# Kernel tuning notes

Measured on AMD Instinct MI355X. Metric: run time of the kernel, lower is better.

Reference implementation:

```python
import jax, jax.numpy as jnp
import numpy as np

FX, FY, CX, CY = 300.0, 300.0, 128.0, 128.0
W, H = 256, 256
NEAR, FAR = 0.01, 100.0
MAX_RADIUS = 64.0
N_GAUSS = 512


def _quat_to_rot(q):
    # (N,4) wxyz quaternion -> (N,3,3) rotation matrix
    q = q / jnp.linalg.norm(q, axis=-1, keepdims=True)
    w, x, y, z = q[..., 0], q[..., 1], q[..., 2], q[..., 3]
    R = jnp.stack([1 - 2 * y * y - 2 * z * z, 2 * x * y - 2 * w * z, 2 * x * z + 2 * w * y,
                   2 * x * y + 2 * w * z, 1 - 2 * x * x - 2 * z * z, 2 * y * z - 2 * w * x,
                   2 * x * z - 2 * w * y, 2 * y * z + 2 * w * x, 1 - 2 * x * x - 2 * y * y], axis=-1)
    return R.reshape(q.shape[:-1] + (3, 3))


def _render(positions, scales, rotations, colors, opacities, view_matrix):
    N = positions.shape[0]
    homo = jnp.concatenate([positions, jnp.ones((N, 1), positions.dtype)], axis=1)
    pc = jnp.einsum('ij,nj->ni', view_matrix, homo)[:, :3]  # camera-space points
    depths = -pc[:, 2]
    R = _quat_to_rot(rotations)
    S = jnp.eye(3, dtype=scales.dtype)[None] * scales[:, None, :]  # diag_embed
    RS = jnp.einsum('ij,njk,nkl->nil', view_matrix[:3, :3], R, S)
    cov3d = RS @ jnp.swapaxes(RS, -1, -2)
    x, y, z = pc[:, 0], pc[:, 1], pc[:, 2]
    z_safe = jnp.maximum(jnp.abs(z), 0.01) * jnp.sign(z + 1e-8)
    z2 = z_safe * z_safe
    zero = jnp.zeros_like(z)
    # Jacobian of perspective projection (N,2,3), signs as in the torch source
    J = jnp.stack([jnp.stack([FX / -z_safe, zero, FX * x / z2], axis=-1),
                   jnp.stack([zero, FY / z_safe, FY * y / z2], axis=-1)], axis=1)
    cov2d = jnp.einsum('nij,njk,nlk->nil', J, cov3d, J)
    u = FX * x / -z_safe + CX
    v = FY * -y / -z_safe + CY
    mx, my = u, v
    # effective radius: 3 * sqrt(max eigenvalue), clamped
    a, b = cov2d[:, 0, 0], cov2d[:, 0, 1]
    c, d = cov2d[:, 1, 0], cov2d[:, 1, 1]
    trace = a + d
    det = jnp.maximum(a * d - b * c, 1e-6)
    disc = jnp.maximum(trace * trace - 4 * det, 0.0)
    lam = (trace + jnp.sqrt(disc)) / 2
    radii = jnp.minimum(3.0 * jnp.sqrt(jnp.maximum(lam, 1e-6)), MAX_RADIUS)
    # front-to-back depth sort
    order = jnp.argsort(depths)
    mx, my = mx[order], my[order]
    cov2d = cov2d[order]
    colors_s = colors[order]
    opac_s = opacities[order]
    depths_s = depths[order]
    radii_s = radii[order]
    visible = ((depths_s > NEAR) & (depths_s < FAR)
               & (mx + radii_s > 0) & (mx - radii_s < W)
               & (my + radii_s > 0) & (my - radii_s < H))
    cov_reg = cov2d + 1e-4 * jnp.eye(2, dtype=cov2d.dtype)
    ra, rb = cov_reg[:, 0, 0], cov_reg[:, 0, 1]
    rc, rd = cov_reg[:, 1, 0], cov_reg[:, 1, 1]
    rdet = ra * rd - rb * rc
    ia, ib, ic, id_ = rd / rdet, -rb / rdet, -rc / rdet, ra / rdet
    px = jnp.arange(W, dtype=jnp.float32)
    py = jnp.arange(H, dtype=jnp.float32)
    # per-Gaussian bounding window, matching torch int() truncation
    x0 = jnp.maximum(0.0, jnp.trunc(mx - radii_s))
    x1 = jnp.minimum(float(W), jnp.trunc(mx + radii_s) + 1.0)
    y0 = jnp.maximum(0.0, jnp.trunc(my - radii_s))
    y1 = jnp.minimum(float(H), jnp.trunc(my + radii_s) + 1.0)
    in_x = (px[None, :] >= x0[:, None]) & (px[None, :] < x1[:, None])  # (N,W)
    in_y = (py[None, :] >= y0[:, None]) & (py[None, :] < y1[:, None])  # (N,H)
    mask = in_y[:, :, None] & in_x[:, None, :] & visible[:, None, None]  # (N,H,W)
    dx = px[None, None, :] - mx[:, None, None]  # (N,1,W)->(N,H,W) broadcast
    dy = py[None, :, None] - my[:, None, None]
    m = (ia[:, None, None] * dx * dx + (ib + ic)[:, None, None] * dx * dy
         + id_[:, None, None] * dy * dy)
    gauss = jnp.exp(-0.5 * m)
    alpha = jnp.where(mask, jnp.clip(opac_s[:, None, None] * gauss, 0.0, 0.99), 0.0)
    # over-compositing: weight_i = alpha_i * prod_{j<i}(1 - alpha_j)
    T = jnp.concatenate([jnp.ones((1, H, W), alpha.dtype),
                         jnp.cumprod(1.0 - alpha, axis=0)[:-1]], axis=0)
    wgt = alpha * T
    img = jnp.einsum('nhw,nc->chw', wgt, colors_s)
    bg = jnp.zeros((3,), img.dtype)  # background = (0,0,0)
    img = img + bg[:, None, None] * (1.0 - jnp.sum(wgt, axis=0))[None]
    return img  # (3,H,W)


def setup_inputs() -> dict:
    key = jax.random.key(0)
    k = jax.random.split(key, 6)
    xy = jax.random.uniform(k[0], (N_GAUSS, 2), minval=-3.0, maxval=3.0)
    z = jax.random.uniform(k[1], (N_GAUSS, 1), minval=-10.0, maxval=-2.0)  # in front of camera
    positions = jnp.concatenate([xy, z], axis=1)
    scales = jax.random.uniform(k[2], (N_GAUSS, 3), minval=0.02, maxval=0.15)
    rotations = jax.random.normal(k[3], (N_GAUSS, 4))
    colors = jax.random.uniform(k[4], (N_GAUSS, 3))
    opacities = jax.random.uniform(k[5], (N_GAUSS,), minval=0.05, maxval=0.95)
    view_matrix = jnp.eye(4, dtype=jnp.float32)
    return {"positions": positions, "scales": scales, "rotations": rotations,
            "colors": colors, "opacities": opacities, "view_matrix": view_matrix}


def reference(positions, scales, rotations, colors, opacities, view_matrix):
    return _render(positions, scales, rotations, colors, opacities, view_matrix)
```

## Files before the change

kernel.cpp:

```cpp
#include <hip/hip_runtime.h>
#include <math.h>

#define NG     512
#define IMG_W  256
#define IMG_H  256
#define FXc    300.0f
#define FYc    300.0f
#define CXc    128.0f
#define CYc    128.0f
#define NEARc  0.01f
#define FARc   100.0f
#define MAXR   64.0f

struct GParam {
  float mx, my, ia, ibc;
  float idv, opac, cr, cg;
  float cb, x0, x1, y0;
  float y1, depth, pad1, pad2;
};

__device__ __forceinline__ unsigned int ordered_float(float f) {
  unsigned int u = __float_as_uint(f);
  return (u & 0x80000000u) ? ~u : (u | 0x80000000u);
}

__global__ __launch_bounds__(256) void fused_render_kernel(
    const float* __restrict__ pos, const float* __restrict__ scl,
    const float* __restrict__ rot, const float* __restrict__ col,
    const float* __restrict__ opa, const float* __restrict__ vm,
    float* __restrict__ out)
{
  __shared__ GParam sg[NG];
  __shared__ unsigned long long keys[NG];
  __shared__ short order[NG];
  __shared__ int wave_cnt[4];

  const int t = threadIdx.x;
  const int wid = t >> 6;
  const int lane = t & 63;

  float V[12];
#pragma unroll
  for (int k = 0; k < 12; ++k) V[k] = vm[k];

#pragma unroll
  for (int chunk = 0; chunk < NG / 256; ++chunk) {
    const int i = chunk * 256 + t;

    const float p0 = pos[i*3+0], p1 = pos[i*3+1], p2 = pos[i*3+2];
    const float pcx = V[0]*p0 + V[1]*p1 + V[2]*p2  + V[3];
    const float pcy = V[4]*p0 + V[5]*p1 + V[6]*p2  + V[7];
    const float pcz = V[8]*p0 + V[9]*p1 + V[10]*p2 + V[11];
    const float depth = -pcz;

    float qw = rot[i*4+0], qx = rot[i*4+1], qy = rot[i*4+2], qz = rot[i*4+3];
    const float qinv = 1.f / sqrtf(qw*qw + qx*qx + qy*qy + qz*qz);
    qw *= qinv; qx *= qinv; qy *= qinv; qz *= qinv;
    const float r00 = 1.f - 2.f*(qy*qy + qz*qz);
    const float r01 = 2.f*(qx*qy - qw*qz);
    const float r02 = 2.f*(qx*qz + qw*qy);
    const float r10 = 2.f*(qx*qy + qw*qz);
    const float r11 = 1.f - 2.f*(qx*qx + qz*qz);
    const float r12 = 2.f*(qy*qz - qw*qx);
    const float r20 = 2.f*(qx*qz - qw*qy);
    const float r21 = 2.f*(qy*qz + qw*qx);
    const float r22 = 1.f - 2.f*(qx*qx + qy*qy);

    const float s0 = scl[i*3+0], s1 = scl[i*3+1], s2 = scl[i*3+2];

    const float m00 = V[0]*r00 + V[1]*r10 + V[2]*r20;
    const float m01 = V[0]*r01 + V[1]*r11 + V[2]*r21;
    const float m02 = V[0]*r02 + V[1]*r12 + V[2]*r22;
    const float m10 = V[4]*r00 + V[5]*r10 + V[6]*r20;
    const float m11 = V[4]*r01 + V[5]*r11 + V[6]*r21;
    const float m12 = V[4]*r02 + V[5]*r12 + V[6]*r22;
    const float m20 = V[8]*r00 + V[9]*r10 + V[10]*r20;
    const float m21 = V[8]*r01 + V[9]*r11 + V[10]*r21;
    const float m22 = V[8]*r02 + V[9]*r12 + V[10]*r22;

    const float a0 = m00*s0, a1 = m01*s1, a2 = m02*s2;
    const float b0 = m10*s0, b1 = m11*s1, b2 = m12*s2;
    const float c0 = m20*s0, c1 = m21*s1, c2 = m22*s2;
    const float c00 = a0*a0 + a1*a1 + a2*a2;
    const float c01 = a0*b0 + a1*b1 + a2*b2;
    const float c02 = a0*c0 + a1*c1 + a2*c2;
    const float c11 = b0*b0 + b1*b1 + b2*b2;
    const float c12 = b0*c0 + b1*c1 + b2*c2;
    const float c22 = c0*c0 + c1*c1 + c2*c2;

    const float zp = pcz + 1e-8f;
    const float sgn = (zp > 0.f) ? 1.f : ((zp < 0.f) ? -1.f : 0.f);
    const float z_safe = fmaxf(fabsf(pcz), 0.01f) * sgn;
    const float z2 = z_safe * z_safe;

    const float j00 = FXc / (-z_safe);
    const float j02 = FXc * pcx / z2;
    const float j11 = FYc / z_safe;
    const float j12 = FYc * pcy / z2;

    const float t00 = j00*c00 + j02*c02;
    const float t01 = j00*c01 + j02*c12;
    const float t02 = j00*c02 + j02*c22;
    const float t10 = j11*c01 + j12*c02;
    const float t11 = j11*c11 + j12*c12;
    const float t12 = j11*c12 + j12*c22;
    const float ca  = t00*j00 + t02*j02;
    const float cbv = t01*j11 + t02*j12;
    const float cc  = t10*j00 + t12*j02;
    const float cd  = t11*j11 + t12*j12;

    const float nz = -z_safe;
    const float u = FXc * pcx / nz + CXc;
    const float v = FYc * (-pcy) / nz + CYc;

    const float trace = ca + cd;
    const float det = fmaxf(ca*cd - cbv*cc, 1e-6f);
    const float disc = fmaxf(trace*trace - 4.f*det, 0.f);
    const float lam = (trace + sqrtf(disc)) * 0.5f;
    const float radii = fminf(3.f * sqrtf(fmaxf(lam, 1e-6f)), MAXR);

    const bool visible = (depth > NEARc) && (depth < FARc) &&
                         (u + radii > 0.f) && (u - radii < (float)IMG_W) &&
                         (v + radii > 0.f) && (v - radii < (float)IMG_H);

    const float ra = ca + 1e-4f;
    const float rb = cbv;
    const float rc = cc;
    const float rd = cd + 1e-4f;
    const float rdet = ra*rd - rb*rc;

    float x0 = fmaxf(0.f, truncf(u - radii));
    float x1 = fminf((float)IMG_W, truncf(u + radii) + 1.f);
    float y0 = fmaxf(0.f, truncf(v - radii));
    float y1 = fminf((float)IMG_H, truncf(v + radii) + 1.f);
    if (!visible) { x0 = 1e9f; x1 = -1e9f; y0 = 1e9f; y1 = -1e9f; }

    GParam g;
    g.mx = u; g.my = v; g.ia = rd / rdet; g.ibc = -(rb + rc) / rdet;
    g.idv = ra / rdet; g.opac = opa[i]; g.cr = col[i*3+0]; g.cg = col[i*3+1];
    g.cb = col[i*3+2]; g.x0 = x0; g.x1 = x1; g.y0 = y0;
    g.y1 = y1; g.depth = depth; g.pad1 = 0.f; g.pad2 = 0.f;
    sg[i] = g;
  }
  __syncthreads();

  const int tileX = blockIdx.x % (IMG_W / 16);
  const int tileY = blockIdx.x / (IMG_W / 16);
  const float tx0 = (float)(tileX * 16), tx1 = tx0 + 16.f;
  const float ty0 = (float)(tileY * 16), ty1 = ty0 + 16.f;

  const int base = wid * 128;
  const int g0 = base + lane;
  const int g1 = base + 64 + lane;
  const bool p0 = (sg[g0].x0 < tx1) & (sg[g0].x1 > tx0) &
                  (sg[g0].y0 < ty1) & (sg[g0].y1 > ty0);
  const bool p1 = (sg[g1].x0 < tx1) & (sg[g1].x1 > tx0) &
                  (sg[g1].y0 < ty1) & (sg[g1].y1 > ty0);
  const unsigned long long mb0 = __ballot(p0);
  const unsigned long long mb1 = __ballot(p1);
  const int pc0 = __popcll(mb0);
  if (lane == 0) wave_cnt[wid] = pc0 + __popcll(mb1);
  __syncthreads();

  int off = 0, total = 0;
#pragma unroll
  for (int w = 0; w < 4; ++w) {
    const int c = wave_cnt[w];
    if (w < wid) off += c;
    total += c;
  }
  const unsigned long long lmask = (1ull << lane) - 1ull;
  if (p0) {
    keys[off + __popcll(mb0 & lmask)] =
        ((unsigned long long)ordered_float(sg[g0].depth) << 32) | (unsigned int)g0;
  }
  if (p1) {
    keys[off + pc0 + __popcll(mb1 & lmask)] =
        ((unsigned long long)ordered_float(sg[g1].depth) << 32) | (unsigned int)g1;
  }
  __syncthreads();

  for (int j = t; j < total; j += 256) {
    const unsigned long long kj = keys[j];
    int rank = 0;
    int i = 0;
    for (; i + 4 <= total; i += 4) {
      rank += (keys[i]   < kj);
      rank += (keys[i+1] < kj);
      rank += (keys[i+2] < kj);
      rank += (keys[i+3] < kj);
    }
    for (; i < total; ++i) rank += (keys[i] < kj);
    order[rank] = (short)(kj & 0xFFFFull);
  }
  __syncthreads();

  const int lx = t & 15, ly = t >> 4;
  const int px = tileX * 16 + lx;
  const int py = tileY * 16 + ly;
  const float fpx = (float)px, fpy = (float)py;

  float T = 1.f, accr = 0.f, accg = 0.f, accb = 0.f;

  for (int k = 0; k < total; ++k) {
    const int n = (int)order[k];
    const float dx = fpx - sg[n].mx;
    const float dy = fpy - sg[n].my;
    const float m = sg[n].ia*dx*dx + sg[n].ibc*dx*dy + sg[n].idv*dy*dy;
    const float g = __expf(-0.5f * m);
    const bool in = (fpx >= sg[n].x0) & (fpx < sg[n].x1) &
                    (fpy >= sg[n].y0) & (fpy < sg[n].y1);
    float a = fminf(sg[n].opac * g, 0.99f);
    a = in ? a : 0.f;
    const float w = a * T;
    accr = fmaf(w, sg[n].cr, accr);
    accg = fmaf(w, sg[n].cg, accg);
    accb = fmaf(w, sg[n].cb, accb);
    T *= (1.f - a);
  }

  const int pix = py * IMG_W + px;
  out[0*IMG_W*IMG_H + pix] = accr;
  out[1*IMG_W*IMG_H + pix] = accg;
  out[2*IMG_W*IMG_H + pix] = accb;
}

extern "C" void kernel_launch(void* const* d_in, const int* in_sizes, int n_in,
                              void* d_out, int out_size, void* d_ws, size_t ws_size,
                              hipStream_t stream) {
  const float* pos = (const float*)d_in[0];
  const float* scl = (const float*)d_in[1];
  const float* rot = (const float*)d_in[2];
  const float* col = (const float*)d_in[3];
  const float* opa = (const float*)d_in[4];
  const float* vm  = (const float*)d_in[5];

  const int tiles = (IMG_W / 16) * (IMG_H / 16);
  fused_render_kernel<<<tiles, 256, 0, stream>>>(pos, scl, rot, col, opa, vm,
                                                 (float*)d_out);
}
```

Baseline: 12.35 us.

## Split per-pixel blending across four threads with shuffle-based compositing merge

Launches 1024-thread blocks so each pixel is handled by four threads, each compositing a contiguous quarter of the depth-sorted Gaussian list. The partial color and transmittance are merged with xor shuffles using the associative front-to-back over operator. Preprocessing and sorting become one-Gaussian-per-thread. This targets the long serial per-pixel loop and low wave occupancy, at the cost of more threads and shuffle merges, with half the block idle during preprocessing.

```diff
diff --git a/kernel.cpp b/kernel.cpp
--- a/kernel.cpp
+++ b/kernel.cpp
@@ -24,7 +24,7 @@
   return (u & 0x80000000u) ? ~u : (u | 0x80000000u);
 }
 
-__global__ __launch_bounds__(256) void fused_render_kernel(
+__global__ __launch_bounds__(1024, 4) void fused_render_kernel(
     const float* __restrict__ pos, const float* __restrict__ scl,
     const float* __restrict__ rot, const float* __restrict__ col,
     const float* __restrict__ opa, const float* __restrict__ vm,
@@ -33,7 +33,7 @@
   __shared__ GParam sg[NG];
   __shared__ unsigned long long keys[NG];
   __shared__ short order[NG];
-  __shared__ int wave_cnt[4];
+  __shared__ int wave_cnt[8];
 
   const int t = threadIdx.x;
   const int wid = t >> 6;
@@ -43,9 +43,8 @@
 #pragma unroll
   for (int k = 0; k < 12; ++k) V[k] = vm[k];
 
-#pragma unroll
-  for (int chunk = 0; chunk < NG / 256; ++chunk) {
-    const int i = chunk * 256 + t;
+  if (t < NG) {
+    const int i = t;
 
     const float p0 = pos[i*3+0], p1 = pos[i*3+1], p2 = pos[i*3+2];
     const float pcx = V[0]*p0 + V[1]*p1 + V[2]*p2  + V[3];
@@ -149,39 +148,34 @@
   const float tx0 = (float)(tileX * 16), tx1 = tx0 + 16.f;
   const float ty0 = (float)(tileY * 16), ty1 = ty0 + 16.f;
 
-  const int base = wid * 128;
-  const int g0 = base + lane;
-  const int g1 = base + 64 + lane;
-  const bool p0 = (sg[g0].x0 < tx1) & (sg[g0].x1 > tx0) &
-                  (sg[g0].y0 < ty1) & (sg[g0].y1 > ty0);
-  const bool p1 = (sg[g1].x0 < tx1) & (sg[g1].x1 > tx0) &
-                  (sg[g1].y0 < ty1) & (sg[g1].y1 > ty0);
-  const unsigned long long mb0 = __ballot(p0);
-  const unsigned long long mb1 = __ballot(p1);
-  const int pc0 = __popcll(mb0);
-  if (lane == 0) wave_cnt[wid] = pc0 + __popcll(mb1);
+  bool pred = false;
+  unsigned long long mb = 0;
+  if (wid < 8) {
+    const int g = wid * 64 + lane;
+    pred = (sg[g].x0 < tx1) & (sg[g].x1 > tx0) &
+           (sg[g].y0 < ty1) & (sg[g].y1 > ty0);
+    mb = __ballot(pred);
+    if (lane == 0) wave_cnt[wid] = __popcll(mb);
+  }
   __syncthreads();
 
   int off = 0, total = 0;
 #pragma unroll
-  for (int w = 0; w < 4; ++w) {
+  for (int w = 0; w < 8; ++w) {
     const int c = wave_cnt[w];
     if (w < wid) off += c;
     total += c;
   }
-  const unsigned long long lmask = (1ull << lane) - 1ull;
-  if (p0) {
-    keys[off + __popcll(mb0 & lmask)] =
-        ((unsigned long long)ordered_float(sg[g0].depth) << 32) | (unsigned int)g0;
-  }
-  if (p1) {
-    keys[off + pc0 + __popcll(mb1 & lmask)] =
-        ((unsigned long long)ordered_float(sg[g1].depth) << 32) | (unsigned int)g1;
-  }
-  __syncthreads();
-
-  for (int j = t; j < total; j += 256) {
-    const unsigned long long kj = keys[j];
+  if (pred) {
+    const int g = wid * 64 + lane;
+    const int p = off + __popcll(mb & ((1ull << lane) - 1ull));
+    keys[p] = ((unsigned long long)ordered_float(sg[g].depth) << 32)
+            | (unsigned int)g;
+  }
+  __syncthreads();
+
+  if (t < total) {
+    const unsigned long long kj = keys[t];
     int rank = 0;
     int i = 0;
     for (; i + 4 <= total; i += 4) {
@@ -195,14 +189,20 @@
   }
   __syncthreads();
 
-  const int lx = t & 15, ly = t >> 4;
+  const int p = t >> 2;
+  const int seg = t & 3;
+  const int lx = p & 15, ly = p >> 4;
   const int px = tileX * 16 + lx;
   const int py = tileY * 16 + ly;
   const float fpx = (float)px, fpy = (float)py;
 
+  const int L = (total + 3) >> 2;
+  const int k0 = seg * L;
+  const int k1 = min(k0 + L, total);
+
   float T = 1.f, accr = 0.f, accg = 0.f, accb = 0.f;
 
-  for (int k = 0; k < total; ++k) {
+  for (int k = k0; k < k1; ++k) {
     const int n = (int)order[k];
     const float dx = fpx - sg[n].mx;
     const float dy = fpy - sg[n].my;
@@ -219,10 +219,30 @@
     T *= (1.f - a);
   }
 
-  const int pix = py * IMG_W + px;
-  out[0*IMG_W*IMG_H + pix] = accr;
-  out[1*IMG_W*IMG_H + pix] = accg;
-  out[2*IMG_W*IMG_H + pix] = accb;
+  {
+    float pT = __shfl_xor(T, 1);
+    float pr = __shfl_xor(accr, 1);
+    float pg = __shfl_xor(accg, 1);
+    float pb = __shfl_xor(accb, 1);
+    if (seg & 1) { accr = pr + pT*accr; accg = pg + pT*accg; accb = pb + pT*accb; }
+    else         { accr = accr + T*pr;  accg = accg + T*pg;  accb = accb + T*pb; }
+    T *= pT;
+
+    pT = __shfl_xor(T, 2);
+    pr = __shfl_xor(accr, 2);
+    pg = __shfl_xor(accg, 2);
+    pb = __shfl_xor(accb, 2);
+    if (seg & 2) { accr = pr + pT*accr; accg = pg + pT*accg; accb = pb + pT*accb; }
+    else         { accr = accr + T*pr;  accg = accg + T*pg;  accb = accb + T*pb; }
+    T *= pT;
+  }
+
+  if (seg == 0) {
+    const int pix = py * IMG_W + px;
+    out[0*IMG_W*IMG_H + pix] = accr;
+    out[1*IMG_W*IMG_H + pix] = accg;
+    out[2*IMG_W*IMG_H + pix] = accb;
+  }
 }
 
 extern "C" void kernel_launch(void* const* d_in, const int* in_sizes, int n_in,
@@ -236,6 +256,6 @@
   const float* vm  = (const float*)d_in[5];
 
   const int tiles = (IMG_W / 16) * (IMG_H / 16);
-  fused_render_kernel<<<tiles, 256, 0, stream>>>(pos, scl, rot, col, opa, vm,
-                                                 (float*)d_out);
+  fused_render_kernel<<<tiles, 1024, 0, stream>>>(pos, scl, rot, col, opa, vm,
+                                                  (float*)d_out);
 }
```

Result: faster. 11.83 us (-4.2%).
